# Kernel tuning notes

Hardware: AMD Instinct MI355X
Metric: run time of the kernel (lower is better)

The kernel has to match this reference:

```python
import jax, jax.numpy as jnp
import numpy as np
from jax import lax

B, C, H, W = 8, 512, 48, 48
E = 512          # embed_dim (== in_channels, required by GLoR fusion channel math)
P = 128          # ContextBlock planes = int(512*0.25)
NC = 2           # num_classes; also used (buggily, but faithfully) as BGAM threshold
TOPK_RATIO = 0.1


def conv1x1(x, w, b=None):
    # w: [out, in]
    y = jnp.einsum('bchw,oc->bohw', x, w)
    if b is not None:
        y = y + b[None, :, None, None]
    return y


def conv3x3(x, w, b):
    y = lax.conv_general_dilated(x, w, (1, 1), 'SAME',
                                 dimension_numbers=('NCHW', 'OIHW', 'NCHW'))
    return y + b[None, :, None, None]


def dwconv3x3(x, w):
    # depthwise: w [C,1,3,3], feature_group_count=C
    return lax.conv_general_dilated(x, w, (1, 1), 'SAME',
                                    dimension_numbers=('NCHW', 'OIHW', 'NCHW'),
                                    feature_group_count=x.shape[1])


def bn_eval(x, g, b):
    # eval-mode BatchNorm2d, running_mean=0, running_var=1, eps=1e-5
    scale = g / jnp.sqrt(1.0 + 1e-5)
    return x * scale[None, :, None, None] + b[None, :, None, None]


def chan_mlp(c, w1, b1, g, bl, w2, b2):
    # ContextBlock channel transform: 1x1 conv -> LayerNorm([P,1,1]) -> ReLU -> 1x1 conv, on [B,C] vectors
    h = c @ w1.T + b1                                  # [B,P]
    mu = h.mean(-1, keepdims=True)
    var = jnp.var(h, axis=-1, keepdims=True)
    h = (h - mu) / jnp.sqrt(var + 1e-5) * g + bl
    h = jax.nn.relu(h)
    return h @ w2.T + b2                               # [B,C]


def cos_self(t):
    # torch F.cosine_similarity(t, t, dim=1): dot/(max(n,eps)*max(n,eps)), eps=1e-8
    nrm2 = jnp.sum(t * t, axis=1)                      # [B,H,W]
    n = jnp.maximum(jnp.sqrt(nrm2), 1e-8)
    return nrm2 / (n * n)


def setup_inputs() -> dict:
    key = jax.random.key(0)
    ks = iter(jax.random.split(key, 64))
    def nrm(shape, scale):
        return (jax.random.normal(next(ks), shape) * scale).astype(jnp.float32)
    def gma(n):
        return (1.0 + 0.05 * jax.random.normal(next(ks), (n,))).astype(jnp.float32)
    def bta(n):
        return (0.05 * jax.random.normal(next(ks), (n,))).astype(jnp.float32)
    sC = 1.0 / np.sqrt(C)
    return dict(
        x=jax.random.normal(next(ks), (B, C, H, W), jnp.float32),
        # GLoR local ConvBranch
        lb_w1=nrm((E, C), sC), lb_g1=gma(E), lb_b1=bta(E),
        lb_w2=nrm((E, 1, 3, 3), 1.0 / 3.0), lb_g2=gma(E), lb_b2=bta(E),
        lb_w3=nrm((E, E), 1.0 / np.sqrt(E)), lb_g3=gma(E), lb_b3=bta(E),
        # GLoR ContextBlock (att pooling, channel_add + channel_mul)
        cm_w=nrm((1, C), sC), cm_b=bta(1),
        ca_w1=nrm((P, C), sC), ca_b1=bta(P), ca_lg=gma(P), ca_lb=bta(P),
        ca_w2=nrm((C, P), 1.0 / np.sqrt(P)), ca_b2=bta(C),
        cmu_w1=nrm((P, C), sC), cmu_b1=bta(P), cmu_lg=gma(P), cmu_lb=bta(P),
        cmu_w2=nrm((C, P), 1.0 / np.sqrt(P)), cmu_b2=bta(C),
        fu_w=nrm((E, 2 * E), 1.0 / np.sqrt(2 * E)), fu_b=bta(E),
        # heads
        sh_w=nrm((NC, E), 1.0 / np.sqrt(E)), sh_b=bta(NC),
        bh_w=nrm((2, E), 1.0 / np.sqrt(E)), bh_b=bta(2),
        # ReverseAttention
        ra_w1=nrm((2, 2, 3, 3), 1.0 / np.sqrt(18)), ra_b1=bta(2), ra_g1=gma(2), ra_bb1=bta(2),
        ra_w2=nrm((2, 2, 3, 3), 1.0 / np.sqrt(18)), ra_b2=bta(2), ra_g2=gma(2), ra_bb2=bta(2),
        # AGCR (all bias=False)
        q_w=nrm((E // 4, E), 1.0 / np.sqrt(E)), k_w=nrm((E // 4, E), 1.0 / np.sqrt(E)),
        v_w=nrm((E, E), 1.0 / np.sqrt(E)), fin_w=nrm((E, 2 * E), 1.0 / np.sqrt(2 * E)),
    )


def reference(x, lb_w1, lb_g1, lb_b1, lb_w2, lb_g2, lb_b2, lb_w3, lb_g3, lb_b3,
              cm_w, cm_b, ca_w1, ca_b1, ca_lg, ca_lb, ca_w2, ca_b2,
              cmu_w1, cmu_b1, cmu_lg, cmu_lb, cmu_w2, cmu_b2, fu_w, fu_b,
              sh_w, sh_b, bh_w, bh_b,
              ra_w1, ra_b1, ra_g1, ra_bb1, ra_w2, ra_b2, ra_g2, ra_bb2,
              q_w, k_w, v_w, fin_w):
    b_, c_, h_, w_ = x.shape
    N = h_ * w_
    # ---- GLoR: local ConvBranch ----
    t = jax.nn.relu(bn_eval(conv1x1(x, lb_w1), lb_g1, lb_b1))
    t = jax.nn.relu(bn_eval(dwconv3x3(t, lb_w2), lb_g2, lb_b2))
    local = bn_eval(conv1x1(t, lb_w3), lb_g3, lb_b3)
    # ---- GLoR: ContextBlock (att pooling) ----
    xf = x.reshape(b_, c_, N)
    mask = (conv1x1(x, cm_w, cm_b)).reshape(b_, 1, N)
    mask = jax.nn.softmax(mask, axis=2)
    ctx = jnp.einsum('bcn,bn->bc', xf, mask[:, 0, :])              # [B,C]
    mul = jax.nn.sigmoid(chan_mlp(ctx, cmu_w1, cmu_b1, cmu_lg, cmu_lb, cmu_w2, cmu_b2))
    add = chan_mlp(ctx, ca_w1, ca_b1, ca_lg, ca_lb, ca_w2, ca_b2)
    glob = x * mul[:, :, None, None] + add[:, :, None, None]
    gx = conv1x1(jnp.concatenate([local, glob], axis=1), fu_w, fu_b)  # [B,E,H,W]
    # ---- heads ----
    sem = conv1x1(gx, sh_w, sh_b)                                   # [B,NC,H,W]
    bdl = conv1x1(gx, bh_w, bh_b)                                   # [B,2,H,W]
    # ---- ReverseAttention(boundary_logits, sigmoid(boundary_logits)) ----
    wx = bdl * (1.0 - jax.nn.sigmoid(bdl))
    r = jax.nn.relu(bn_eval(conv3x3(wx, ra_w1, ra_b1), ra_g1, ra_bb1))
    r = jax.nn.relu(bn_eval(conv3x3(r, ra_w2, ra_b2), ra_g2, ra_bb2))
    # ---- BGAM (threshold = num_classes, faithful to source) ----
    thr = jnp.float32(NC)
    st = (cos_self(sem) > thr).astype(x.dtype)
    bt = (cos_self(r) > thr).astype(x.dtype)
    region = ((1.0 - st) * (1.0 - bt))[:, None]                     # [B,1,H,W]
    # ---- AGCR custom attention ----
    k_num = int(N * TOPK_RATIO)
    q = conv1x1(gx, q_w).reshape(b_, -1, N)                         # [B,E/4,N]
    kk = conv1x1(gx, k_w).reshape(b_, -1, N)
    v = conv1x1(gx, v_w).reshape(b_, E, N)
    attn = jnp.einsum('bdm,bdn->bmn', q, kk) / jnp.sqrt(jnp.float32(q.shape[1]))
    aw = jax.nn.softmax(attn, axis=-1)                              # [B,N,N]
    topv, _ = lax.top_k(aw, k_num)
    soft = topv.mean(-1)                                            # [B,N]
    aw = aw * soft[:, None, :]
    # bmm(value, aw^T).mean(-1) == value @ aw.mean(rows)
    col_mean = aw.mean(axis=1)                                      # [B,N]
    ctx2 = jnp.einsum('bcn,bn->bc', v, col_mean)                    # [B,E]
    ctx2 = jnp.broadcast_to(ctx2[:, :, None, None], gx.shape)
    refined = jnp.concatenate([gx, ctx2 * region], axis=1)          # [B,2E,H,W]
    return conv1x1(refined, fin_w)                                  # [B,E,H,W]
```

## Files before the change

kernel.cpp:

```cpp
#include <hip/hip_runtime.h>
#include <math.h>

#define NPIX 2304
#define NCH  512
#define NB   8
#define KNUM 230

typedef unsigned short u16;
typedef __attribute__((ext_vector_type(8))) short short8v;
typedef __attribute__((ext_vector_type(4))) float float4v;

__device__ __forceinline__ float bf2f(u16 u) {
    union { unsigned v; float f; } x; x.v = ((unsigned)u) << 16; return x.f;
}
__device__ __forceinline__ u16 f2bf(float f) {
    union { float f; unsigned v; } x; x.f = f;
    unsigned r = x.v + 0x7FFFu + ((x.v >> 16) & 1u);
    return (u16)(r >> 16);
}

__device__ __forceinline__ float waveSum(float v) {
    #pragma unroll
    for (int o = 32; o > 0; o >>= 1) v += __shfl_down(v, o);
    return v;
}
__device__ __forceinline__ float blockSum256(float v, float* sc4) {
    v = waveSum(v);
    __syncthreads();
    if ((threadIdx.x & 63) == 0) sc4[threadIdx.x >> 6] = v;
    __syncthreads();
    return sc4[0] + sc4[1] + sc4[2] + sc4[3];
}
__device__ __forceinline__ float waveMaxF(float v) {
    #pragma unroll
    for (int o = 32; o > 0; o >>= 1) v = fmaxf(v, __shfl_down(v, o));
    return v;
}
__device__ __forceinline__ float blockMax256(float v, float* sc4) {
    v = waveMaxF(v);
    __syncthreads();
    if ((threadIdx.x & 63) == 0) sc4[threadIdx.x >> 6] = v;
    __syncthreads();
    return fmaxf(fmaxf(sc4[0], sc4[1]), fmaxf(sc4[2], sc4[3]));
}

__device__ __forceinline__ void gl_lds16(const u16* g, u16* l) {
    __builtin_amdgcn_global_load_lds(
        reinterpret_cast<const unsigned __attribute__((address_space(1)))*>(
            reinterpret_cast<uintptr_t>(g)),
        reinterpret_cast<unsigned __attribute__((address_space(3)))*>(
            reinterpret_cast<uintptr_t>(l)),
        16, 0, 0);
}

__global__ __launch_bounds__(256, 2) void mfma_gemm(
    const u16* __restrict__ A, int ldA, long sA,
    const u16* __restrict__ B0, const u16* __restrict__ B1, int ldB, long sB,
    void* __restrict__ outp, int ldO, long sO,
    const float* __restrict__ scaleR, const float* __restrict__ biasR,
    const float* __restrict__ biasC, int ldbc,
    int K, float alpha, int flags)
{
    __shared__ u16 lA[128 * 64];
    __shared__ u16 lB[128 * 64];
    const int t  = threadIdx.x;
    const int w  = t >> 6, l = t & 63;
    const int wR = w >> 1, wC = w & 1;
    const int lg = l >> 4, lr = l & 15, l7 = l & 7;
    const int b   = blockIdx.z;
    const int Cl0 = blockIdx.x * 128;
    const int R0  = blockIdx.y * 128;
    const u16* Ab  = A + (size_t)b * sA;
    const u16* B0b = B0 + (size_t)b * sB;
    const u16* B1b = B1 ? B1 + (size_t)b * sB : nullptr;

    float4v acc[4][4];
    const float4v zero = {0.f, 0.f, 0.f, 0.f};
    #pragma unroll
    for (int i = 0; i < 4; ++i)
        #pragma unroll
        for (int j = 0; j < 4; ++j) acc[i][j] = zero;

    const int sr = t >> 3;
    const int sp = t & 7;

    for (int k0 = 0; k0 < K; k0 += 64) {
        const u16* Bsrc = B0b; int kb = k0;
        if (B1b && k0 >= 512) { Bsrc = B1b; kb = k0 - 512; }
        #pragma unroll
        for (int i = 0; i < 4; ++i) {
            const int r  = i * 32 + sr;
            const int ca = sp ^ (r & 7);
            gl_lds16(Ab   + (size_t)(R0  + r) * ldA + (k0 + ca * 8), &lA[i * 2048 + t * 8]);
            gl_lds16(Bsrc + (size_t)(Cl0 + r) * ldB + (kb + ca * 8), &lB[i * 2048 + t * 8]);
        }
        __syncthreads();
        #pragma unroll
        for (int kk = 0; kk < 2; ++kk) {
            short8v af[4], bfv[4];
            const int p = (kk * 4 + lg) ^ l7;
            #pragma unroll
            for (int mt = 0; mt < 4; ++mt) {
                const int rA = wR * 64 + mt * 16 + lr;
                af[mt]  = *reinterpret_cast<const short8v*>(&lA[rA * 64 + p * 8]);
                const int rB = wC * 64 + mt * 16 + lr;
                bfv[mt] = *reinterpret_cast<const short8v*>(&lB[rB * 64 + p * 8]);
            }
            #pragma unroll
            for (int mt = 0; mt < 4; ++mt)
                #pragma unroll
                for (int nt = 0; nt < 4; ++nt)
                    acc[mt][nt] = __builtin_amdgcn_mfma_f32_16x16x32_bf16(
                        af[mt], bfv[nt], acc[mt][nt], 0, 0, 0);
        }
        __syncthreads();
    }

    const bool relu = (flags & 1), f32o = (flags & 2);
    #pragma unroll
    for (int nt = 0; nt < 4; ++nt) {
        const int Cl = Cl0 + wC * 64 + nt * 16 + lr;
        const float bc = biasC ? biasC[(size_t)b * ldbc + Cl] : 0.f;
        #pragma unroll
        for (int mt = 0; mt < 4; ++mt) {
            const int Rb = R0 + wR * 64 + mt * 16 + lg * 4;
            float4 scv = scaleR ? *reinterpret_cast<const float4*>(&scaleR[Rb])
                                : make_float4(1.f, 1.f, 1.f, 1.f);
            float4 bv  = biasR  ? *reinterpret_cast<const float4*>(&biasR[Rb])
                                : make_float4(0.f, 0.f, 0.f, 0.f);
            float vals[4];
            #pragma unroll
            for (int j = 0; j < 4; ++j) {
                const float sc = alpha * ((&scv.x)[j]);
                float v = acc[mt][nt][j] * sc + (&bv.x)[j] + bc;
                if (relu) v = fmaxf(v, 0.f);
                vals[j] = v;
            }
            if (f32o) {
                float* op = (float*)outp + (size_t)b * sO + (size_t)Cl * ldO + Rb;
                *reinterpret_cast<float4*>(op) = make_float4(vals[0], vals[1], vals[2], vals[3]);
            } else {
                ushort4 u;
                u.x = f2bf(vals[0]); u.y = f2bf(vals[1]);
                u.z = f2bf(vals[2]); u.w = f2bf(vals[3]);
                u16* op = (u16*)outp + (size_t)b * sO + (size_t)Cl * ldO + Rb;
                *reinterpret_cast<ushort4*>(op) = u;
            }
        }
    }
}

__global__ __launch_bounds__(256) void transpose_cvt(
    const float* __restrict__ x, u16* __restrict__ xb)
{
    __shared__ float tile[64][65];
    const int t = threadIdx.x;
    const int n0 = blockIdx.x * 64, c0 = blockIdx.y * 64, b = blockIdx.z;
    const int tr = t >> 4, tc4 = (t & 15) * 4;
    #pragma unroll
    for (int i = 0; i < 4; ++i) {
        const int cc = tr + i * 16;
        float4 v = *reinterpret_cast<const float4*>(
            x + ((size_t)(b * NCH + c0 + cc)) * NPIX + n0 + tc4);
        tile[cc][tc4 + 0] = v.x; tile[cc][tc4 + 1] = v.y;
        tile[cc][tc4 + 2] = v.z; tile[cc][tc4 + 3] = v.w;
    }
    __syncthreads();
    #pragma unroll
    for (int i = 0; i < 4; ++i) {
        const int nn = tr + i * 16;
        ushort4 u;
        u.x = f2bf(tile[tc4 + 0][nn]); u.y = f2bf(tile[tc4 + 1][nn]);
        u.z = f2bf(tile[tc4 + 2][nn]); u.w = f2bf(tile[tc4 + 3][nn]);
        *reinterpret_cast<ushort4*>(xb + ((size_t)b * NPIX + n0 + nn) * NCH + c0 + tc4) = u;
    }
}

__global__ __launch_bounds__(256) void cvt_bf16(
    const float* __restrict__ s, u16* __restrict__ d, int n4)
{
    const int i = blockIdx.x * 256 + threadIdx.x;
    if (i < n4) {
        float4 v = reinterpret_cast<const float4*>(s)[i];
        ushort4 u; u.x = f2bf(v.x); u.y = f2bf(v.y); u.z = f2bf(v.z); u.w = f2bf(v.w);
        reinterpret_cast<ushort4*>(d)[i] = u;
    }
}

__global__ __launch_bounds__(256) void fold_dw(
    const float* __restrict__ wsrc, const float* __restrict__ g, float* __restrict__ wf)
{
    const int i = blockIdx.x * 256 + threadIdx.x;
    if (i < 9 * NCH) {
        const int c = i / 9, tap = i % 9;
        wf[tap * NCH + c] = wsrc[i] * g[c] * 0.99999500003749978f;
    }
}

__global__ __launch_bounds__(256) void dwconv_k(
    const u16* __restrict__ t1, const float* __restrict__ wf,
    const float* __restrict__ b2, u16* __restrict__ t2)
{
    const int idx = blockIdx.x * 256 + threadIdx.x;
    const int cq = idx & 127;
    const int n  = (idx >> 7) % NPIX;
    const int b  = (idx >> 7) / NPIX;
    const int c  = cq * 4;
    const int y = n / 48, x = n % 48;
    float s0 = 0.f, s1 = 0.f, s2 = 0.f, s3 = 0.f;
    #pragma unroll
    for (int dy = -1; dy <= 1; ++dy) {
        const int yy = y + dy;
        if (yy < 0 || yy >= 48) continue;
        #pragma unroll
        for (int dx = -1; dx <= 1; ++dx) {
            const int xx = x + dx;
            if (xx < 0 || xx >= 48) continue;
            ushort4 tv = *reinterpret_cast<const ushort4*>(
                &t1[((size_t)b * NPIX + yy * 48 + xx) * NCH + c]);
            float4 wv = *reinterpret_cast<const float4*>(
                &wf[((dy + 1) * 3 + dx + 1) * NCH + c]);
            s0 = fmaf(bf2f(tv.x), wv.x, s0); s1 = fmaf(bf2f(tv.y), wv.y, s1);
            s2 = fmaf(bf2f(tv.z), wv.z, s2); s3 = fmaf(bf2f(tv.w), wv.w, s3);
        }
    }
    float4 bb = *reinterpret_cast<const float4*>(&b2[c]);
    ushort4 o;
    o.x = f2bf(fmaxf(s0 + bb.x, 0.f)); o.y = f2bf(fmaxf(s1 + bb.y, 0.f));
    o.z = f2bf(fmaxf(s2 + bb.z, 0.f)); o.w = f2bf(fmaxf(s3 + bb.w, 0.f));
    *reinterpret_cast<ushort4*>(&t2[((size_t)b * NPIX + n) * NCH + c]) = o;
}

__global__ __launch_bounds__(256) void mask_logits_k(
    const u16* __restrict__ xb, const float* __restrict__ cmw,
    const float* __restrict__ cmb, float* __restrict__ logits)
{
    const int w = threadIdx.x >> 6, l = threadIdx.x & 63;
    const int n = blockIdx.x * 4 + w, b = blockIdx.y;
    const ushort4* row = reinterpret_cast<const ushort4*>(xb + ((size_t)b * NPIX + n) * NCH);
    const int c0 = l * 8;
    ushort4 u0 = row[l * 2], u1 = row[l * 2 + 1];
    float4 w0 = *reinterpret_cast<const float4*>(&cmw[c0]);
    float4 w1 = *reinterpret_cast<const float4*>(&cmw[c0 + 4]);
    float s = bf2f(u0.x) * w0.x + bf2f(u0.y) * w0.y + bf2f(u0.z) * w0.z + bf2f(u0.w) * w0.w
            + bf2f(u1.x) * w1.x + bf2f(u1.y) * w1.y + bf2f(u1.z) * w1.z + bf2f(u1.w) * w1.w;
    s = waveSum(s);
    if (l == 0) logits[(size_t)b * NPIX + n] = s + cmb[0];
}

__global__ __launch_bounds__(256) void softmax_mask(
    const float* __restrict__ logits, float* __restrict__ mask)
{
    __shared__ float sc[4];
    const int b = blockIdx.x, t = threadIdx.x;
    const float* lr = logits + (size_t)b * NPIX;
    float mx = -3.4e38f;
    for (int i = t; i < NPIX; i += 256) mx = fmaxf(mx, lr[i]);
    mx = blockMax256(mx, sc);
    float s = 0.f;
    for (int i = t; i < NPIX; i += 256) s += __expf(lr[i] - mx);
    s = blockSum256(s, sc);
    const float inv = 1.0f / s;
    for (int i = t; i < NPIX; i += 256) mask[(size_t)b * NPIX + i] = __expf(lr[i] - mx) * inv;
}

__global__ __launch_bounds__(512) void ctx_pool_k(
    const u16* __restrict__ xb, const float* __restrict__ mask, float* __restrict__ ctx)
{
    const int c = threadIdx.x, b = blockIdx.y;
    const int nn0 = blockIdx.x * 128;
    float s = 0.f;
    for (int n = nn0; n < nn0 + 128; ++n)
        s = fmaf(bf2f(xb[((size_t)b * NPIX + n) * NCH + c]), mask[(size_t)b * NPIX + n], s);
    atomicAdd(&ctx[b * NCH + c], s);
}

__global__ __launch_bounds__(128) void chan_mlps(
    const float* __restrict__ ctxv,
    const float* __restrict__ mw1, const float* __restrict__ mb1,
    const float* __restrict__ mlg, const float* __restrict__ mlb,
    const float* __restrict__ mw2, const float* __restrict__ mb2,
    const float* __restrict__ aw1, const float* __restrict__ ab1,
    const float* __restrict__ alg, const float* __restrict__ alb,
    const float* __restrict__ aw2, const float* __restrict__ ab2,
    float* __restrict__ mulo, float* __restrict__ addo)
{
    __shared__ float cs[512];
    __shared__ float hm[128], ha[128];
    __shared__ float sc[2];
    const int b = blockIdx.x, t = threadIdx.x;
    for (int i = t; i < 512; i += 128) cs[i] = ctxv[b * 512 + i];
    __syncthreads();
    float hmv = mb1[t], hav = ab1[t];
    for (int c = 0; c < 512; ++c) {
        const float cv = cs[c];
        hmv = fmaf(cv, mw1[t * 512 + c], hmv);
        hav = fmaf(cv, aw1[t * 512 + c], hav);
    }
    {
        float s1 = waveSum(hmv);
        __syncthreads();
        if ((t & 63) == 0) sc[t >> 6] = s1;
        __syncthreads();
        const float mu = (sc[0] + sc[1]) * (1.0f / 128.0f);
        const float d = hmv - mu;
        float s2 = waveSum(d * d);
        __syncthreads();
        if ((t & 63) == 0) sc[t >> 6] = s2;
        __syncthreads();
        const float var = (sc[0] + sc[1]) * (1.0f / 128.0f);
        hm[t] = fmaxf(d / sqrtf(var + 1e-5f) * mlg[t] + mlb[t], 0.f);
    }
    {
        float s1 = waveSum(hav);
        __syncthreads();
        if ((t & 63) == 0) sc[t >> 6] = s1;
        __syncthreads();
        const float mu = (sc[0] + sc[1]) * (1.0f / 128.0f);
        const float d = hav - mu;
        float s2 = waveSum(d * d);
        __syncthreads();
        if ((t & 63) == 0) sc[t >> 6] = s2;
        __syncthreads();
        const float var = (sc[0] + sc[1]) * (1.0f / 128.0f);
        ha[t] = fmaxf(d / sqrtf(var + 1e-5f) * alg[t] + alb[t], 0.f);
    }
    __syncthreads();
    for (int o = t; o < 512; o += 128) {
        float sm = mb2[o], sa = ab2[o];
        for (int p = 0; p < 128; ++p) {
            sm = fmaf(hm[p], mw2[o * 128 + p], sm);
            sa = fmaf(ha[p], aw2[o * 128 + p], sa);
        }
        mulo[b * 512 + o] = 1.0f / (1.0f + __expf(-sm));
        addo[b * 512 + o] = sa;
    }
}

__global__ __launch_bounds__(256) void glob_ew_k(
    const u16* __restrict__ xb, const float* __restrict__ mulv,
    const float* __restrict__ addv, u16* __restrict__ g)
{
    const int idx = blockIdx.x * 256 + threadIdx.x;
    const int cq = idx & 63;
    const int n = (idx >> 6) % NPIX;
    const int b = (idx >> 6) / NPIX;
    const int c = cq * 8;
    const size_t base = ((size_t)b * NPIX + n) * NCH + c;
    ushort4 u0 = *reinterpret_cast<const ushort4*>(&xb[base]);
    ushort4 u1 = *reinterpret_cast<const ushort4*>(&xb[base + 4]);
    const float* mp = &mulv[b * NCH + c];
    const float* ap = &addv[b * NCH + c];
    float4 m0 = *reinterpret_cast<const float4*>(mp);
    float4 m1 = *reinterpret_cast<const float4*>(mp + 4);
    float4 a0 = *reinterpret_cast<const float4*>(ap);
    float4 a1 = *reinterpret_cast<const float4*>(ap + 4);
    ushort4 o0, o1;
    o0.x = f2bf(fmaf(bf2f(u0.x), m0.x, a0.x));
    o0.y = f2bf(fmaf(bf2f(u0.y), m0.y, a0.y));
    o0.z = f2bf(fmaf(bf2f(u0.z), m0.z, a0.z));
    o0.w = f2bf(fmaf(bf2f(u0.w), m0.w, a0.w));
    o1.x = f2bf(fmaf(bf2f(u1.x), m1.x, a1.x));
    o1.y = f2bf(fmaf(bf2f(u1.y), m1.y, a1.y));
    o1.z = f2bf(fmaf(bf2f(u1.z), m1.z, a1.z));
    o1.w = f2bf(fmaf(bf2f(u1.w), m1.w, a1.w));
    *reinterpret_cast<ushort4*>(&g[base]) = o0;
    *reinterpret_cast<ushort4*>(&g[base + 4]) = o1;
}

__global__ __launch_bounds__(256) void softmax_topk_wave(
    const u16* __restrict__ p, float* __restrict__ mxo,
    float* __restrict__ invSo, float* __restrict__ softo, int bOff)
{
    const int w = threadIdx.x >> 6, l = threadIdx.x & 63;
    const int r = blockIdx.x * 4 + w;
    const int bc = blockIdx.y;
    const u16* pr = p + ((size_t)bc * NPIX + r) * NPIX;
    float e[36];
    float mx = -3.4e38f;
    #pragma unroll
    for (int i = 0; i < 36; ++i) { e[i] = bf2f(pr[i * 64 + l]); mx = fmaxf(mx, e[i]); }
    #pragma unroll
    for (int o = 32; o > 0; o >>= 1) mx = fmaxf(mx, __shfl_xor(mx, o));
    float S = 0.f;
    #pragma unroll
    for (int i = 0; i < 36; ++i) { e[i] = __expf(e[i] - mx); S += e[i]; }
    #pragma unroll
    for (int o = 32; o > 0; o >>= 1) S += __shfl_xor(S, o);
    const float invS = 1.0f / S;
    unsigned lo = 0u, hi = 0x3F800000u;
    while (lo < hi) {
        const unsigned mid = lo + ((hi - lo + 1u) >> 1);
        const float tv = __uint_as_float(mid);
        int c = 0;
        #pragma unroll
        for (int i = 0; i < 36; ++i)
            c += (int)__popcll(__ballot(e[i] >= tv));
        if (c >= KNUM) lo = mid; else hi = mid - 1u;
    }
    const float tv = __uint_as_float(lo);
    float ss = 0.f; int a = 0;
    #pragma unroll
    for (int i = 0; i < 36; ++i) {
        if (e[i] > tv) ss += e[i];
        a += (int)__popcll(__ballot(e[i] > tv));
    }
    #pragma unroll
    for (int o = 32; o > 0; o >>= 1) ss += __shfl_xor(ss, o);
    if (l == 0) {
        const size_t gi = (size_t)(bOff + bc) * NPIX + r;
        mxo[gi] = mx; invSo[gi] = invS;
        softo[gi] = (ss + (float)(KNUM - a) * tv) * invS * (1.0f / (float)KNUM);
    }
}

__global__ __launch_bounds__(256) void colsum_k(
    const u16* __restrict__ p, const float* __restrict__ mxo,
    const float* __restrict__ invSo, float* __restrict__ colsum, int bOff)
{
    const int j = blockIdx.x * 256 + threadIdx.x;
    const int ic0 = blockIdx.y * 72;
    const int bc = blockIdx.z;
    const float* mxr = mxo + (size_t)(bOff + bc) * NPIX;
    const float* isr = invSo + (size_t)(bOff + bc) * NPIX;
    const u16* pb = p + (size_t)bc * NPIX * NPIX;
    float s = 0.f;
    #pragma unroll 4
    for (int i = ic0; i < ic0 + 72; ++i)
        s += __expf(bf2f(pb[(size_t)i * NPIX + j]) - mxr[i]) * isr[i];
    atomicAdd(&colsum[(size_t)(bOff + bc) * NPIX + j], s);
}

__global__ __launch_bounds__(512) void ctx2_pool_k(
    const u16* __restrict__ qkv, const float* __restrict__ colsum,
    const float* __restrict__ soft, float* __restrict__ ctx2)
{
    const int c = threadIdx.x, b = blockIdx.y;
    const int nn0 = blockIdx.x * 128;
    float s = 0.f;
    for (int n = nn0; n < nn0 + 128; ++n) {
        const float wgt = colsum[(size_t)b * NPIX + n] * soft[(size_t)b * NPIX + n];
        s = fmaf(bf2f(qkv[((size_t)b * NPIX + n) * 768 + 256 + c]), wgt, s);
    }
    atomicAdd(&ctx2[b * NCH + c], s * (1.0f / (float)NPIX));
}

__global__ __launch_bounds__(256) void compute_z(
    const float* __restrict__ finw, const float* __restrict__ ctx2, float* __restrict__ z)
{
    const int o = blockIdx.x * 256 + threadIdx.x;
    const int b = blockIdx.y;
    const float* c2 = ctx2 + b * NCH;
    const float* wr = finw + (size_t)o * 1024 + 512;
    float s = 0.f;
    for (int c = 0; c < NCH; ++c) s = fmaf(wr[c], c2[c], s);
    z[b * NCH + o] = s;
}

extern "C" void kernel_launch(void* const* d_in, const int* in_sizes, int n_in,
                              void* d_out, int out_size, void* d_ws, size_t ws_size,
                              hipStream_t stream)
{
    (void)in_sizes; (void)n_in; (void)out_size; (void)ws_size;
    const float* x      = (const float*)d_in[0];
    const float* lb_w1  = (const float*)d_in[1];
    const float* lb_g1  = (const float*)d_in[2];
    const float* lb_b1  = (const float*)d_in[3];
    const float* lb_w2  = (const float*)d_in[4];
    const float* lb_g2  = (const float*)d_in[5];
    const float* lb_b2  = (const float*)d_in[6];
    const float* lb_w3  = (const float*)d_in[7];
    const float* lb_g3  = (const float*)d_in[8];
    const float* lb_b3  = (const float*)d_in[9];
    const float* cm_w   = (const float*)d_in[10];
    const float* cm_b   = (const float*)d_in[11];
    const float* ca_w1  = (const float*)d_in[12];
    const float* ca_b1  = (const float*)d_in[13];
    const float* ca_lg  = (const float*)d_in[14];
    const float* ca_lb  = (const float*)d_in[15];
    const float* ca_w2  = (const float*)d_in[16];
    const float* ca_b2  = (const float*)d_in[17];
    const float* cmu_w1 = (const float*)d_in[18];
    const float* cmu_b1 = (const float*)d_in[19];
    const float* cmu_lg = (const float*)d_in[20];
    const float* cmu_lb = (const float*)d_in[21];
    const float* cmu_w2 = (const float*)d_in[22];
    const float* cmu_b2 = (const float*)d_in[23];
    const float* fu_w   = (const float*)d_in[24];
    const float* fu_b   = (const float*)d_in[25];
    const float* q_w    = (const float*)d_in[38];
    const float* k_w    = (const float*)d_in[39];
    const float* v_w    = (const float*)d_in[40];
    const float* fin_w  = (const float*)d_in[41];

    char* W = (char*)d_ws;
    const size_t SZ_ACT = (size_t)NB * NPIX * NCH * 2;
    u16* xb   = (u16*)(W);
    u16* bufA = (u16*)(W + SZ_ACT);
    u16* bufB = (u16*)(W + 2 * SZ_ACT);
    u16* gx   = (u16*)(W + 3 * SZ_ACT);
    u16* qkv  = (u16*)(W + 4 * SZ_ACT);
    char* SM = W + 4 * SZ_ACT + (size_t)NB * NPIX * 768 * 2;
    float* logits = (float*)SM; SM += (size_t)NB * NPIX * 4;
    float* maskb  = (float*)SM; SM += (size_t)NB * NPIX * 4;
    float* mxb    = (float*)SM; SM += (size_t)NB * NPIX * 4;
    float* invSb  = (float*)SM; SM += (size_t)NB * NPIX * 4;
    float* softb  = (float*)SM; SM += (size_t)NB * NPIX * 4;
    float* colsum = (float*)SM; SM += (size_t)NB * NPIX * 4;
    float* ctxb   = (float*)SM; SM += (size_t)NB * NCH * 4;
    float* ctx2b  = (float*)SM; SM += (size_t)NB * NCH * 4;
    float* mulb   = (float*)SM; SM += (size_t)NB * NCH * 4;
    float* addb   = (float*)SM; SM += (size_t)NB * NCH * 4;
    float* zbuf   = (float*)SM; SM += (size_t)NB * NCH * 4;
    float* wfold  = (float*)SM; SM += (size_t)9 * NCH * 4;
    u16* w1b   = (u16*)SM; SM += (size_t)512 * 512 * 2;
    u16* w3b   = (u16*)SM; SM += (size_t)512 * 512 * 2;
    u16* fuwb  = (u16*)SM; SM += (size_t)512 * 1024 * 2;
    u16* finwb = (u16*)SM; SM += (size_t)512 * 1024 * 2;
    u16* qkvwb = (u16*)SM; SM += (size_t)768 * 512 * 2;
    u16* pbuf = xb;

    const float invs  = 0.99999500003749978f;
    const float rs128 = 0.08838834764831845f;
    const long SACT = (long)NPIX * NCH;

    cvt_bf16<<<256, 256, 0, stream>>>(lb_w1, w1b, 65536);
    cvt_bf16<<<256, 256, 0, stream>>>(lb_w3, w3b, 65536);
    cvt_bf16<<<512, 256, 0, stream>>>(fu_w, fuwb, 131072);
    cvt_bf16<<<512, 256, 0, stream>>>(fin_w, finwb, 131072);
    cvt_bf16<<<64, 256, 0, stream>>>(q_w, qkvwb, 16384);
    cvt_bf16<<<64, 256, 0, stream>>>(k_w, qkvwb + 128 * 512, 16384);
    cvt_bf16<<<256, 256, 0, stream>>>(v_w, qkvwb + 256 * 512, 65536);
    fold_dw<<<18, 256, 0, stream>>>(lb_w2, lb_g2, wfold);
    transpose_cvt<<<dim3(36, 8, 8), 256, 0, stream>>>(x, xb);
    hipMemsetAsync(colsum, 0, (size_t)NB * NPIX * 4 + 2 * (size_t)NB * NCH * 4, stream);

    mfma_gemm<<<dim3(18, 4, 8), 256, 0, stream>>>(w1b, 512, 0, xb, nullptr, 512, SACT,
        bufA, 512, SACT, lb_g1, lb_b1, nullptr, 0, 512, invs, 1);
    dwconv_k<<<9216, 256, 0, stream>>>(bufA, wfold, lb_b2, bufB);
    mfma_gemm<<<dim3(18, 4, 8), 256, 0, stream>>>(w3b, 512, 0, bufB, nullptr, 512, SACT,
        bufA, 512, SACT, lb_g3, lb_b3, nullptr, 0, 512, invs, 0);
    mask_logits_k<<<dim3(576, 8), 256, 0, stream>>>(xb, cm_w, cm_b, logits);
    softmax_mask<<<8, 256, 0, stream>>>(logits, maskb);
    ctx_pool_k<<<dim3(18, 8), 512, 0, stream>>>(xb, maskb, ctxb);
    chan_mlps<<<8, 128, 0, stream>>>(ctxb,
        cmu_w1, cmu_b1, cmu_lg, cmu_lb, cmu_w2, cmu_b2,
        ca_w1, ca_b1, ca_lg, ca_lb, ca_w2, ca_b2, mulb, addb);
    glob_ew_k<<<4608, 256, 0, stream>>>(xb, mulb, addb, bufB);
    mfma_gemm<<<dim3(18, 4, 8), 256, 0, stream>>>(fuwb, 1024, 0, bufA, bufB, 512, SACT,
        gx, 512, SACT, nullptr, fu_b, nullptr, 0, 1024, 1.0f, 0);
    mfma_gemm<<<dim3(18, 6, 8), 256, 0, stream>>>(qkvwb, 512, 0, gx, nullptr, 512, SACT,
        qkv, 768, (long)NPIX * 768, nullptr, nullptr, nullptr, 0, 512, 1.0f, 0);
    for (int cc = 0; cc < 2; ++cc) {
        const u16* kp = qkv + (size_t)cc * 4 * NPIX * 768 + 128;
        const u16* qp = qkv + (size_t)cc * 4 * NPIX * 768;
        mfma_gemm<<<dim3(18, 18, 4), 256, 0, stream>>>(kp, 768, (long)NPIX * 768,
            qp, nullptr, 768, (long)NPIX * 768,
            pbuf, NPIX, (long)NPIX * NPIX, nullptr, nullptr, nullptr, 0, 128, rs128, 0);
        softmax_topk_wave<<<dim3(576, 4), 256, 0, stream>>>(pbuf, mxb, invSb, softb, cc * 4);
        colsum_k<<<dim3(9, 32, 4), 256, 0, stream>>>(pbuf, mxb, invSb, colsum, cc * 4);
    }
    ctx2_pool_k<<<dim3(18, 8), 512, 0, stream>>>(qkv, colsum, softb, ctx2b);
    compute_z<<<dim3(2, 8), 256, 0, stream>>>(fin_w, ctx2b, zbuf);
    mfma_gemm<<<dim3(4, 18, 8), 256, 0, stream>>>(gx, 512, SACT, finwb, nullptr, 1024, 0,
        d_out, NPIX, (long)NCH * NPIX, nullptr, nullptr, zbuf, 512, 512, 1.0f, 2);
}
```

Baseline: 449.2 us.

## Radix-select top-k on bf16 sort keys and parallelize channel MLPs

The softmax/top-k kernel now maps bf16 logits to order-preserving 16-bit integer keys. It finds the k-th largest with a 16-step bitwise radix select instead of a float binary search over exp values of about 30 steps. Exponentials are computed once after the threshold is found, and the loads are vectorized to 16-byte reads. Separately, the channel MLP kernel splits the two paths across blocks, uses coalesced float4 weight reads and wave reductions for the first layer, and doubles the thread count. The threshold is now taken on the logits rather than on the exp values, which should be equivalent because exp is monotonic, but ties and rounding behaviour may differ slightly.

```diff
diff --git a/kernel.cpp b/kernel.cpp
--- a/kernel.cpp
+++ b/kernel.cpp
@@ -275,7 +275,7 @@
     atomicAdd(&ctx[b * NCH + c], s);
 }
 
-__global__ __launch_bounds__(128) void chan_mlps(
+__global__ __launch_bounds__(256) void chan_mlp2(
     const float* __restrict__ ctxv,
     const float* __restrict__ mw1, const float* __restrict__ mb1,
     const float* __restrict__ mlg, const float* __restrict__ mlb,
@@ -286,54 +286,51 @@
     float* __restrict__ mulo, float* __restrict__ addo)
 {
     __shared__ float cs[512];
-    __shared__ float hm[128], ha[128];
-    __shared__ float sc[2];
-    const int b = blockIdx.x, t = threadIdx.x;
-    for (int i = t; i < 512; i += 128) cs[i] = ctxv[b * 512 + i];
-    __syncthreads();
-    float hmv = mb1[t], hav = ab1[t];
-    for (int c = 0; c < 512; ++c) {
-        const float cv = cs[c];
-        hmv = fmaf(cv, mw1[t * 512 + c], hmv);
-        hav = fmaf(cv, aw1[t * 512 + c], hav);
-    }
-    {
-        float s1 = waveSum(hmv);
-        __syncthreads();
-        if ((t & 63) == 0) sc[t >> 6] = s1;
-        __syncthreads();
-        const float mu = (sc[0] + sc[1]) * (1.0f / 128.0f);
-        const float d = hmv - mu;
-        float s2 = waveSum(d * d);
-        __syncthreads();
-        if ((t & 63) == 0) sc[t >> 6] = s2;
-        __syncthreads();
-        const float var = (sc[0] + sc[1]) * (1.0f / 128.0f);
-        hm[t] = fmaxf(d / sqrtf(var + 1e-5f) * mlg[t] + mlb[t], 0.f);
-    }
-    {
-        float s1 = waveSum(hav);
-        __syncthreads();
-        if ((t & 63) == 0) sc[t >> 6] = s1;
-        __syncthreads();
-        const float mu = (sc[0] + sc[1]) * (1.0f / 128.0f);
-        const float d = hav - mu;
-        float s2 = waveSum(d * d);
-        __syncthreads();
-        if ((t & 63) == 0) sc[t >> 6] = s2;
-        __syncthreads();
-        const float var = (sc[0] + sc[1]) * (1.0f / 128.0f);
-        ha[t] = fmaxf(d / sqrtf(var + 1e-5f) * alg[t] + alb[t], 0.f);
-    }
-    __syncthreads();
-    for (int o = t; o < 512; o += 128) {
-        float sm = mb2[o], sa = ab2[o];
-        for (int p = 0; p < 128; ++p) {
-            sm = fmaf(hm[p], mw2[o * 128 + p], sm);
-            sa = fmaf(ha[p], aw2[o * 128 + p], sa);
+    __shared__ float hn[128];
+    __shared__ float sc4[4];
+    const int path = blockIdx.x, b = blockIdx.y;
+    const int t = threadIdx.x, w = t >> 6, l = t & 63;
+    const float* W1 = path ? aw1 : mw1;
+    const float* B1 = path ? ab1 : mb1;
+    const float* LG = path ? alg : mlg;
+    const float* LB = path ? alb : mlb;
+    const float* W2 = path ? aw2 : mw2;
+    const float* B2 = path ? ab2 : mb2;
+    cs[t]       = ctxv[b * 512 + t];
+    cs[t + 256] = ctxv[b * 512 + 256 + t];
+    __syncthreads();
+    const float4 ca = *reinterpret_cast<const float4*>(&cs[l * 8]);
+    const float4 cb = *reinterpret_cast<const float4*>(&cs[l * 8 + 4]);
+    #pragma unroll 4
+    for (int hh = 0; hh < 32; ++hh) {
+        const int h = w * 32 + hh;
+        const float4 wa = *reinterpret_cast<const float4*>(&W1[h * 512 + l * 8]);
+        const float4 wb = *reinterpret_cast<const float4*>(&W1[h * 512 + l * 8 + 4]);
+        float s = wa.x * ca.x + wa.y * ca.y + wa.z * ca.z + wa.w * ca.w
+                + wb.x * cb.x + wb.y * cb.y + wb.z * cb.z + wb.w * cb.w;
+        s = waveSum(s);
+        if (l == 0) hn[h] = s + B1[h];
+    }
+    __syncthreads();
+    const float v = (t < 128) ? hn[t] : 0.f;
+    const float s1 = blockSum256(v, sc4);
+    const float mu = s1 * (1.0f / 128.0f);
+    const float d = (t < 128) ? (v - mu) : 0.f;
+    const float s2 = blockSum256(d * d, sc4);
+    const float var = s2 * (1.0f / 128.0f);
+    if (t < 128) hn[t] = fmaxf(d / sqrtf(var + 1e-5f) * LG[t] + LB[t], 0.f);
+    __syncthreads();
+    #pragma unroll
+    for (int oo = 0; oo < 2; ++oo) {
+        const int o = t + oo * 256;
+        float s = B2[o];
+        #pragma unroll
+        for (int p = 0; p < 128; p += 4) {
+            const float4 wv = *reinterpret_cast<const float4*>(&W2[o * 128 + p]);
+            s += wv.x * hn[p] + wv.y * hn[p + 1] + wv.z * hn[p + 2] + wv.w * hn[p + 3];
         }
-        mulo[b * 512 + o] = 1.0f / (1.0f + __expf(-sm));
-        addo[b * 512 + o] = sa;
+        if (path == 0) mulo[b * 512 + o] = 1.0f / (1.0f + __expf(-s));
+        else           addo[b * 512 + o] = s;
     }
 }
 
@@ -376,41 +373,55 @@
     const int r = blockIdx.x * 4 + w;
     const int bc = blockIdx.y;
     const u16* pr = p + ((size_t)bc * NPIX + r) * NPIX;
-    float e[36];
-    float mx = -3.4e38f;
-    #pragma unroll
-    for (int i = 0; i < 36; ++i) { e[i] = bf2f(pr[i * 64 + l]); mx = fmaxf(mx, e[i]); }
-    #pragma unroll
-    for (int o = 32; o > 0; o >>= 1) mx = fmaxf(mx, __shfl_xor(mx, o));
-    float S = 0.f;
-    #pragma unroll
-    for (int i = 0; i < 36; ++i) { e[i] = __expf(e[i] - mx); S += e[i]; }
-    #pragma unroll
-    for (int o = 32; o > 0; o >>= 1) S += __shfl_xor(S, o);
-    const float invS = 1.0f / S;
-    unsigned lo = 0u, hi = 0x3F800000u;
-    while (lo < hi) {
-        const unsigned mid = lo + ((hi - lo + 1u) >> 1);
-        const float tv = __uint_as_float(mid);
+    const uint4* p16 = reinterpret_cast<const uint4*>(pr);
+    uint4 q0 = p16[l], q1 = p16[64 + l], q2 = p16[128 + l], q3 = p16[192 + l];
+    uint2 q4 = reinterpret_cast<const uint2*>(pr)[512 + l];
+    unsigned uw[18] = {q0.x, q0.y, q0.z, q0.w, q1.x, q1.y, q1.z, q1.w,
+                       q2.x, q2.y, q2.z, q2.w, q3.x, q3.y, q3.z, q3.w,
+                       q4.x, q4.y};
+    unsigned km[36];
+    #pragma unroll
+    for (int i = 0; i < 18; ++i) {
+        const unsigned v = uw[i];
+        const unsigned m = ((v >> 15) & 0x10001u) * 0x7FFFu + 0x80008000u;
+        const unsigned s = v ^ m;
+        km[2 * i]     = s & 0xFFFFu;
+        km[2 * i + 1] = s >> 16;
+    }
+    unsigned kmax = km[0];
+    #pragma unroll
+    for (int i = 1; i < 36; ++i) kmax = max(kmax, km[i]);
+    #pragma unroll
+    for (int o = 32; o > 0; o >>= 1) kmax = max(kmax, (unsigned)__shfl_xor((int)kmax, o));
+    const unsigned mxbits = (kmax & 0x8000u) ? (kmax ^ 0x8000u) : (kmax ^ 0xFFFFu);
+    const float mx = bf2f((u16)mxbits);
+    unsigned kt = 0u;
+    for (int bit = 15; bit >= 0; --bit) {
+        const unsigned cand = kt | (1u << bit);
         int c = 0;
         #pragma unroll
         for (int i = 0; i < 36; ++i)
-            c += (int)__popcll(__ballot(e[i] >= tv));
-        if (c >= KNUM) lo = mid; else hi = mid - 1u;
-    }
-    const float tv = __uint_as_float(lo);
-    float ss = 0.f; int a = 0;
+            c += (int)__popcll(__ballot(km[i] >= cand));
+        if (c >= KNUM) kt = cand;
+    }
+    const unsigned tbits = (kt & 0x8000u) ? (kt ^ 0x8000u) : (kt ^ 0xFFFFu);
+    const float te = __expf(bf2f((u16)tbits) - mx);
+    float S = 0.f, ss = 0.f; int a = 0;
     #pragma unroll
     for (int i = 0; i < 36; ++i) {
-        if (e[i] > tv) ss += e[i];
-        a += (int)__popcll(__ballot(e[i] > tv));
-    }
-    #pragma unroll
-    for (int o = 32; o > 0; o >>= 1) ss += __shfl_xor(ss, o);
+        const unsigned bb = (km[i] & 0x8000u) ? (km[i] ^ 0x8000u) : (km[i] ^ 0xFFFFu);
+        const float e = __expf(bf2f((u16)bb) - mx);
+        S += e;
+        const bool gt = km[i] > kt;
+        if (gt) ss += e;
+        a += (int)__popcll(__ballot(gt));
+    }
+    #pragma unroll
+    for (int o = 32; o > 0; o >>= 1) { S += __shfl_xor(S, o); ss += __shfl_xor(ss, o); }
     if (l == 0) {
         const size_t gi = (size_t)(bOff + bc) * NPIX + r;
-        mxo[gi] = mx; invSo[gi] = invS;
-        softo[gi] = (ss + (float)(KNUM - a) * tv) * invS * (1.0f / (float)KNUM);
+        mxo[gi] = mx; invSo[gi] = 1.0f / S;
+        softo[gi] = (ss + (float)(KNUM - a) * te) / (S * (float)KNUM);
     }
 }
 
@@ -543,7 +554,7 @@
     mask_logits_k<<<dim3(576, 8), 256, 0, stream>>>(xb, cm_w, cm_b, logits);
     softmax_mask<<<8, 256, 0, stream>>>(logits, maskb);
     ctx_pool_k<<<dim3(18, 8), 512, 0, stream>>>(xb, maskb, ctxb);
-    chan_mlps<<<8, 128, 0, stream>>>(ctxb,
+    chan_mlp2<<<dim3(2, 8), 256, 0, stream>>>(ctxb,
         cmu_w1, cmu_b1, cmu_lg, cmu_lb, cmu_w2, cmu_b2,
         ca_w1, ca_b1, ca_lg, ca_lb, ca_w2, ca_b2, mulb, addb);
     glob_ew_k<<<4608, 256, 0, stream>>>(xb, mulb, addb, bufB);
```

Measured after the change: 402.7 us. 10.3% less time.
